# Kernel tuning notes

Hardware: AMD Instinct MI355X
Metric: run time of the kernel (lower is better)

Reference implementation:

```python
import jax, jax.numpy as jnp
import numpy as np

N = 100000
E = 3200000
D_IN = 128
D_OUT = 128


def setup_inputs() -> dict:
    key = jax.random.key(0)
    k1, k2, k3, k4, k5, k6, k7 = jax.random.split(key, 7)
    stdv = 1.0 / np.sqrt(D_OUT)
    x = jax.random.normal(k1, (N, D_IN), dtype=jnp.float32)
    rows = jax.random.randint(k2, (E,), 0, N, dtype=jnp.int32)
    cols = jax.random.randint(k3, (E,), 0, N, dtype=jnp.int32)
    edge_w = jax.random.uniform(k4, (E,), dtype=jnp.float32)
    W = jax.random.uniform(k5, (D_IN, D_OUT), minval=-stdv, maxval=stdv, dtype=jnp.float32)
    W_skip = jax.random.uniform(k6, (D_IN, D_OUT), minval=-stdv, maxval=stdv, dtype=jnp.float32)
    b = jax.random.uniform(k7, (D_OUT,), minval=-stdv, maxval=stdv, dtype=jnp.float32)
    return {"x": x, "rows": rows, "cols": cols, "edge_w": edge_w,
            "W": W, "W_skip": W_skip, "b": b}


def reference(x, rows, cols, edge_w, W, W_skip, b):
    # support1 = x @ W  [N, D_OUT]
    support1 = jnp.dot(x, W)
    # spmm(norm_adj, support1): out[r] = sum_{(r,c) in E} w_rc * support1[c]
    msgs = support1[cols] * edge_w[:, None]          # [E, D_OUT] gather
    agg = jax.ops.segment_sum(msgs, rows, num_segments=N)  # [N, D_OUT] scatter-add
    # skip connection + bias
    out = agg + jnp.dot(x, W_skip) + b
    return out
```

## Files before the change

### kernel.cpp

```cpp
#include <hip/hip_runtime.h>

#define D 128
#define BP_LOG 7
#define ROWS_H 64
#define MAX_NB 1024
#define GEMM_GRID 784
#define CHUNK_LOG 12
#define CAP 2560

typedef short bf16x8 __attribute__((ext_vector_type(8)));
typedef float f32x4  __attribute__((ext_vector_type(4)));

static __device__ __forceinline__ unsigned short f2bf(float f) {
    unsigned u = __float_as_uint(f);
    u += 0x7FFFu + ((u >> 16) & 1u);
    return (unsigned short)(u >> 16);
}

__global__ __launch_bounds__(256) void wconv_kernel(
    const float* __restrict__ W, const float* __restrict__ Ws,
    short* __restrict__ Wt, int* __restrict__ bhist, int nb)
{
    const int idx = blockIdx.x * 256 + threadIdx.x;
    if (idx < 2 * D * D) {
        const int mat = idx >> 14;
        const int rem = idx & (D * D - 1);
        const int n = rem >> 7, k = rem & (D - 1);
        const float* src = mat ? Ws : W;
        Wt[idx] = (short)f2bf(src[k * D + n]);
    }
    if (idx < nb) bhist[idx] = 0;
}

__global__ __launch_bounds__(256) void bhist_kernel(
    const int* __restrict__ rows, int* __restrict__ bhist, int E, int nb)
{
    __shared__ int h[MAX_NB];
    const int t = threadIdx.x;
    for (int i = t; i < nb; i += 256) h[i] = 0;
    __syncthreads();

    int i = blockIdx.x * 256 + t;
    const int stride = gridDim.x * 256;
    for (; i < E; i += stride) atomicAdd(&h[rows[i] >> BP_LOG], 1);
    __syncthreads();

    for (int i2 = t; i2 < nb; i2 += 256) {
        const int c = h[i2];
        if (c) atomicAdd(&bhist[i2], c);
    }
}

__global__ __launch_bounds__(256) void bscan_kernel(
    const int* __restrict__ bhist, int* __restrict__ bptr,
    int* __restrict__ bcur, int nb)
{
    const int t = threadIdx.x;
    const int base_i = t * 4;
    int v[4];
    int s = 0;
#pragma unroll
    for (int k = 0; k < 4; ++k) {
        v[k] = (base_i + k < nb) ? bhist[base_i + k] : 0;
        s += v[k];
    }

    const int lane = t & 63, wv = t >> 6;
    int sc = s;
    for (int o = 1; o < 64; o <<= 1) {
        const int u = __shfl_up(sc, o, 64);
        if (lane >= o) sc += u;
    }
    __shared__ int wsum[4];
    if (lane == 63) wsum[wv] = sc;
    __syncthreads();

    int wbase = 0;
    for (int w2 = 0; w2 < wv; ++w2) wbase += wsum[w2];
    int excl = wbase + (sc - s);
#pragma unroll
    for (int k = 0; k < 4; ++k) {
        if (base_i + k < nb) { bptr[base_i + k] = excl; bcur[base_i + k] = excl; }
        excl += v[k];
    }
    if (t == 255) bptr[nb] = wsum[0] + wsum[1] + wsum[2] + wsum[3];
}

__global__ __launch_bounds__(256) void gemm_part_kernel(
    const float* __restrict__ x, const short* __restrict__ Wt,
    const float* __restrict__ b, unsigned short* __restrict__ s1b,
    unsigned short* __restrict__ skipb, int N,
    const int* __restrict__ rows, const int* __restrict__ cols,
    const float* __restrict__ ew, int* __restrict__ bcur,
    int2* __restrict__ se1, int E, int nb)
{
    __shared__ short sx[64 * D];

    const int t = threadIdx.x;

    if (blockIdx.x >= GEMM_GRID) {
        int* h = (int*)sx;
        const int nbl = gridDim.x - GEMM_GRID;
        const int nchunks = (E + (1 << CHUNK_LOG) - 1) >> CHUNK_LOG;

        for (int c = blockIdx.x - GEMM_GRID; c < nchunks; c += nbl) {
            const int ebeg = c << CHUNK_LOG;
            const int eend = min(ebeg + (1 << CHUNK_LOG), E);

            for (int i = t; i < nb; i += 256) h[i] = 0;
            __syncthreads();

            for (int e = ebeg + t; e < eend; e += 256)
                atomicAdd(&h[rows[e] >> BP_LOG], 1);
            __syncthreads();

            for (int i = t; i < nb; i += 256) {
                const int cnt = h[i];
                h[i] = cnt ? atomicAdd(&bcur[i], cnt) : 0;
            }
            __syncthreads();

            for (int e = ebeg + t; e < eend; e += 256) {
                const int r    = rows[e];
                const int bkt  = r >> BP_LOG;
                const int slot = atomicAdd(&h[bkt], 1);
                se1[slot] = make_int2(((r & 127) << 20) | cols[e],
                                      __float_as_int(ew[e]));
            }
            __syncthreads();
        }
        return;
    }

    const int lane = t & 63;
    const int w    = t >> 6;

    const int bmat = w >> 1;
    const int bn0  = (w & 1) * 64 + (lane & 15);
    const int bk0  = (lane >> 4) * 8;
    bf16x8 Bf[4][4];
#pragma unroll
    for (int nf = 0; nf < 4; ++nf)
#pragma unroll
        for (int ks = 0; ks < 4; ++ks)
            Bf[nf][ks] = *(const bf16x8*)&Wt[
                ((size_t)bmat * D + bn0 + nf * 16) * D + ks * 32 + bk0];

    float bias[4];
#pragma unroll
    for (int nf = 0; nf < 4; ++nf)
        bias[nf] = (w >= 2) ? b[(w - 2) * 64 + nf * 16 + (lane & 15)] : 0.f;

    const int ntiles = (N + 63) >> 6;
    const int trow = t >> 2;
    const int tk   = (t & 3) * 4;

    for (int rt = blockIdx.x; rt < ntiles; rt += GEMM_GRID) {
        const int r0 = rt << 6;
        __syncthreads();

        const int grow = min(r0 + trow, N - 1);
        const float* xrow = &x[(size_t)grow * D];
#pragma unroll
        for (int i = 0; i < 8; ++i) {
            const int k = tk + i * 16;
            const float4 v = *(const float4*)&xrow[k];
            const unsigned lo = (unsigned)f2bf(v.x) | ((unsigned)f2bf(v.y) << 16);
            const unsigned hi = (unsigned)f2bf(v.z) | ((unsigned)f2bf(v.w) << 16);
            unsigned byte = trow * 256 + k * 2;
            byte ^= (unsigned)((trow & 7) << 4);
            *(uint2*)((char*)sx + byte) = make_uint2(lo, hi);
        }
        __syncthreads();

        f32x4 acc[4][4];
#pragma unroll
        for (int mf = 0; mf < 4; ++mf)
#pragma unroll
            for (int nf = 0; nf < 4; ++nf)
                acc[mf][nf] = (f32x4){0.f, 0.f, 0.f, 0.f};

#pragma unroll
        for (int ks = 0; ks < 4; ++ks) {
            bf16x8 Af[4];
#pragma unroll
            for (int mf = 0; mf < 4; ++mf) {
                const int row = mf * 16 + (lane & 15);
                unsigned byte = row * 256 + (ks * 32 + bk0) * 2;
                byte ^= (unsigned)((row & 7) << 4);
                Af[mf] = *(const bf16x8*)((const char*)sx + byte);
            }
#pragma unroll
            for (int mf = 0; mf < 4; ++mf)
#pragma unroll
                for (int nf = 0; nf < 4; ++nf)
                    acc[mf][nf] = __builtin_amdgcn_mfma_f32_16x16x32_bf16(
                        Af[mf], Bf[nf][ks], acc[mf][nf], 0, 0, 0);
        }

#pragma unroll
        for (int mf = 0; mf < 4; ++mf) {
#pragma unroll
            for (int i = 0; i < 4; ++i) {
                const int row = r0 + mf * 16 + (lane >> 4) * 4 + i;
                if (row < N) {
                    if (w < 2) {
#pragma unroll
                        for (int nf = 0; nf < 4; ++nf) {
                            const int col = w * 64 + nf * 16 + (lane & 15);
                            s1b[(size_t)row * D + col] = f2bf(acc[mf][nf][i]);
                        }
                    } else {
#pragma unroll
                        for (int nf = 0; nf < 4; ++nf) {
                            const int col = (w - 2) * 64 + nf * 16 + (lane & 15);
                            skipb[(size_t)row * D + col] =
                                f2bf(acc[mf][nf][i] + bias[nf]);
                        }
                    }
                }
            }
        }
    }
}

__global__ __launch_bounds__(512) void sortspmm_kernel(
    const unsigned short* __restrict__ s1b,
    const unsigned short* __restrict__ skipb,
    const int* __restrict__ bptr, const int2* __restrict__ se1,
    float* __restrict__ out, int N)
{
    __shared__ long long recs[CAP];
    __shared__ unsigned short perm[CAP];
    __shared__ int rpos[ROWS_H];
    __shared__ int rcur[ROWS_H];
    __shared__ int nstage;

    const int t    = threadIdx.x;
    const int lane = t & 63;
    const int wv   = t >> 6;
    const int sb   = blockIdx.x >> 1;
    const int hh   = blockIdx.x & 1;
    const int r0   = (sb << BP_LOG) + (hh << 6);
    const int j    = lane * 2;

    const int beg  = bptr[sb];
    const int end  = bptr[sb + 1];
    const long long* seq = (const long long*)se1;

    if (t < ROWS_H) rcur[t] = 0;
    if (t == 0) nstage = 0;
    __syncthreads();

    for (int e = beg + t; e < end; e += 512) {
        const long long rec = seq[e];
        const int rl = (int)((unsigned)rec >> 20);
        const bool m = ((rl >> 6) == hh);
        const unsigned long long bal = __ballot(m);
        if (bal) {
            const int leader = (int)__ffsll((long long)bal) - 1;
            int base = 0;
            if (lane == leader) base = atomicAdd(&nstage, __popcll(bal));
            base = __shfl(base, leader, 64);
            if (m) {
                const int slot = base +
                    (int)__popcll(bal & ((1ull << lane) - 1ull));
                if (slot < CAP) recs[slot] = rec;
            }
        }
    }
    __syncthreads();
    const int hcnt = nstage;

    if (hcnt <= CAP) {
        for (int i = t; i < hcnt; i += 512)
            atomicAdd(&rcur[(int)((unsigned)recs[i] >> 20) & 63], 1);
        __syncthreads();

        if (t < ROWS_H) {
            const int v = rcur[t];
            int sc = v;
#pragma unroll
            for (int o = 1; o < 64; o <<= 1) {
                const int u = __shfl_up(sc, o, 64);
                if (lane >= o) sc += u;
            }
            rpos[t] = sc - v;
            rcur[t] = sc - v;
        }
        __syncthreads();

        for (int i = t; i < hcnt; i += 512) {
            const int rl = (int)((unsigned)recs[i] >> 20) & 63;
            perm[atomicAdd(&rcur[rl], 1)] = (unsigned short)i;
        }
        __syncthreads();

        for (int i2 = 0; i2 < 8; ++i2) {
            const int rr = wv * 8 + i2;
            const int r  = r0 + rr;
            if (r >= N) break;
            int p        = rpos[rr];
            const int pe = rcur[rr];

            float2 acc = make_float2(0.f, 0.f);
            for (; p + 8 <= pe; p += 8) {
                int idx[8];
#pragma unroll
                for (int k = 0; k < 8; ++k) idx[k] = perm[p + k];
                long long ed[8];
#pragma unroll
                for (int k = 0; k < 8; ++k) ed[k] = recs[idx[k]];
                unsigned pk[8];
#pragma unroll
                for (int k = 0; k < 8; ++k)
                    pk[k] = *(const unsigned*)&s1b[
                        (size_t)((unsigned)ed[k] & 0xFFFFFu) * D + j];
#pragma unroll
                for (int k = 0; k < 8; ++k) {
                    const float w = __int_as_float((int)(ed[k] >> 32));
                    acc.x = fmaf(w, __uint_as_float(pk[k] << 16), acc.x);
                    acc.y = fmaf(w, __uint_as_float(pk[k] & 0xFFFF0000u), acc.y);
                }
            }
            for (; p < pe; ++p) {
                const long long ed = recs[perm[p]];
                const unsigned pk = *(const unsigned*)&s1b[
                    (size_t)((unsigned)ed & 0xFFFFFu) * D + j];
                const float w = __int_as_float((int)(ed >> 32));
                acc.x = fmaf(w, __uint_as_float(pk << 16), acc.x);
                acc.y = fmaf(w, __uint_as_float(pk & 0xFFFF0000u), acc.y);
            }

            const unsigned sk = *(const unsigned*)&skipb[(size_t)r * D + j];
            float2 o;
            o.x = acc.x + __uint_as_float(sk << 16);
            o.y = acc.y + __uint_as_float(sk & 0xFFFF0000u);
            *(float2*)&out[(size_t)r * D + j] = o;
        }
    } else {
        const int nr = min(ROWS_H, N - r0);
        for (int idx = t; idx < nr * 64; idx += 512) {
            const int rr = idx >> 6;
            const int cc = (idx & 63) * 2;
            const unsigned sk = *(const unsigned*)&skipb[(size_t)(r0 + rr) * D + cc];
            *(float2*)&out[(size_t)(r0 + rr) * D + cc] =
                make_float2(__uint_as_float(sk << 16),
                            __uint_as_float(sk & 0xFFFF0000u));
        }
        __syncthreads();

        for (int e = beg + wv; e < end; e += 8) {
            const long long ed = seq[e];
            const unsigned key = (unsigned)ed;
            const int rl = (int)(key >> 20);
            if ((rl >> 6) != hh) continue;
            const float w = __int_as_float((int)(ed >> 32));
            const unsigned pk = *(const unsigned*)&s1b[
                (size_t)(key & 0xFFFFFu) * D + j];
            float* op = &out[(size_t)(r0 + (rl & 63)) * D + j];
            unsafeAtomicAdd(op,     w * __uint_as_float(pk << 16));
            unsafeAtomicAdd(op + 1, w * __uint_as_float(pk & 0xFFFF0000u));
        }
    }
}

__global__ __launch_bounds__(512) void dual_gemm_fb_kernel(
    const float* __restrict__ x, const float* __restrict__ W,
    const float* __restrict__ Ws, const float* __restrict__ b,
    unsigned short* __restrict__ s1b, float* __restrict__ out, int N)
{
    __shared__ float sW[D * D];
    __shared__ float sWs[D * D];

    const int t = threadIdx.x;
    for (int i = t * 4; i < D * D; i += 512 * 4) {
        *(float4*)&sW[i]  = *(const float4*)&W[i];
        *(float4*)&sWs[i] = *(const float4*)&Ws[i];
    }
    __syncthreads();

    const int lane   = t & 63;
    const int wave   = blockIdx.x * 8 + (t >> 6);
    const int nwaves = gridDim.x * 8;
    const int j      = lane * 2;
    const float2 bb  = *(const float2*)&b[j];

    for (int r0 = wave * 4; r0 < N; r0 += nwaves * 4) {
        float2 xr[4];
#pragma unroll
        for (int r = 0; r < 4; ++r)
            xr[r] = *(const float2*)&x[(size_t)(r0 + r) * D + j];

        float2 a1[4], a2[4];
#pragma unroll
        for (int r = 0; r < 4; ++r) {
            a1[r] = make_float2(0.f, 0.f);
            a2[r] = make_float2(0.f, 0.f);
        }

#pragma unroll 8
        for (int k = 0; k < D; ++k) {
            const float2 wk  = *(const float2*)&sW[k * D + j];
            const float2 wsk = *(const float2*)&sWs[k * D + j];
#pragma unroll
            for (int r = 0; r < 4; ++r) {
                const float xv = __shfl((k & 1) ? xr[r].y : xr[r].x, k >> 1, 64);
                a1[r].x = fmaf(xv, wk.x,  a1[r].x);
                a1[r].y = fmaf(xv, wk.y,  a1[r].y);
                a2[r].x = fmaf(xv, wsk.x, a2[r].x);
                a2[r].y = fmaf(xv, wsk.y, a2[r].y);
            }
        }

#pragma unroll
        for (int r = 0; r < 4; ++r) {
            const unsigned pk = (unsigned)f2bf(a1[r].x) |
                                ((unsigned)f2bf(a1[r].y) << 16);
            *(unsigned*)&s1b[(size_t)(r0 + r) * D + j] = pk;
            *(float2*)&out[(size_t)(r0 + r) * D + j] =
                make_float2(a2[r].x + bb.x, a2[r].y + bb.y);
        }
    }
}

__global__ __launch_bounds__(256) void spmm_edges_kernel(
    const unsigned short* __restrict__ s1b, const int* __restrict__ rows,
    const int* __restrict__ cols, const float* __restrict__ ew,
    float* __restrict__ out, int E)
{
    const int lane = threadIdx.x & 63;
    const int wave = blockIdx.x * (blockDim.x >> 6) + (threadIdx.x >> 6);
    const int nw   = gridDim.x * (blockDim.x >> 6);
    const int j    = lane * 2;

    const int epw   = (E + nw - 1) / nw;
    const int e_beg = wave * epw;
    const int e_end = min(e_beg + epw, E);

    for (int e = e_beg; e < e_end; ++e) {
        const int   r = rows[e];
        const int   c = cols[e];
        const float w = ew[e];
        const unsigned p = *(const unsigned*)&s1b[(size_t)c * D + j];
        float* o = &out[(size_t)r * D + j];
        unsafeAtomicAdd(o,     w * __uint_as_float(p << 16));
        unsafeAtomicAdd(o + 1, w * __uint_as_float(p & 0xFFFF0000u));
    }
}

extern "C" void kernel_launch(void* const* d_in, const int* in_sizes, int n_in,
                              void* d_out, int out_size, void* d_ws, size_t ws_size,
                              hipStream_t stream) {
    const float* x    = (const float*)d_in[0];
    const int*   rows = (const int*)  d_in[1];
    const int*   cols = (const int*)  d_in[2];
    const float* ew   = (const float*)d_in[3];
    const float* W    = (const float*)d_in[4];
    const float* Ws   = (const float*)d_in[5];
    const float* b    = (const float*)d_in[6];
    float*       out  = (float*)d_out;

    const int N  = in_sizes[0] / D;
    const int E  = in_sizes[1];
    const int nb = (N + 127) >> BP_LOG;

    const size_t s1_bytes   = ((size_t)N * D * 2 + 15) & ~(size_t)15;
    const size_t skip_bytes = s1_bytes;
    const size_t wt_bytes   = (size_t)2 * D * D * 2;
    const size_t int_bytes  = (((size_t)(3 * nb + 1)) * 4 + 7) & ~(size_t)7;
    const size_t need       = s1_bytes + skip_bytes + wt_bytes + int_bytes
                              + (size_t)E * 8;

    unsigned short* s1b = (unsigned short*)d_ws;

    if (ws_size >= need && nb <= MAX_NB) {
        unsigned short* skipb = (unsigned short*)((char*)d_ws + s1_bytes);
        short* Wt    = (short*)((char*)d_ws + s1_bytes + skip_bytes);
        int*   ibase = (int*)((char*)d_ws + s1_bytes + skip_bytes + wt_bytes);
        int*  bhist  = ibase;
        int*  bptr   = ibase + nb;
        int*  bcur   = ibase + 2 * nb + 1;
        int2* se1    = (int2*)((char*)d_ws + s1_bytes + skip_bytes + wt_bytes
                               + int_bytes);

        wconv_kernel<<<(2 * D * D + 255) / 256, 256, 0, stream>>>(W, Ws, Wt, bhist, nb);
        bhist_kernel<<<512, 256, 0, stream>>>(rows, bhist, E, nb);
        bscan_kernel<<<1, 256, 0, stream>>>(bhist, bptr, bcur, nb);

        const int nchunks = (E + (1 << CHUNK_LOG) - 1) >> CHUNK_LOG;
        const int part_blocks = min(nchunks, 1024);
        gemm_part_kernel<<<GEMM_GRID + part_blocks, 256, 0, stream>>>(
            x, Wt, b, s1b, skipb, N, rows, cols, ew, bcur, se1, E, nb);

        sortspmm_kernel<<<nb * 2, 512, 0, stream>>>(s1b, skipb, bptr, se1, out, N);
    } else {
        dual_gemm_fb_kernel<<<768, 512, 0, stream>>>(x, W, Ws, b, s1b, (float*)d_out, N);
        spmm_edges_kernel<<<2048, 256, 0, stream>>>(s1b, rows, cols, ew, (float*)d_out, E);
    }
}
```

Measured before the change: 219.5 us.

## Reorder fused gemm/partition grid, vectorize histogram loads, unroll gather by 16

The fused GEMM+edge-partition kernel now puts the partition blocks first and gives each 64-row GEMM tile its own block instead of looping over a fixed grid, so the latency-bound partition work is dispatched early. The bucket histogram reads rows as int4 to cut load instructions. The SpMM gather loop gains a 16-wide unrolled stage for more loads in flight. The trade-off is more GEMM blocks each reloading the B fragments, and more register pressure in the gather loop.

Result: slower. 230.9 us (+5.2%).

```diff
diff --git a/kernel.cpp b/kernel.cpp
--- a/kernel.cpp
+++ b/kernel.cpp
@@ -4,7 +4,6 @@
 #define BP_LOG 7
 #define ROWS_H 64
 #define MAX_NB 1024
-#define GEMM_GRID 784
 #define CHUNK_LOG 12
 #define CAP 2560
 
@@ -40,9 +39,18 @@
     for (int i = t; i < nb; i += 256) h[i] = 0;
     __syncthreads();
 
+    const int nq = E >> 2;
     int i = blockIdx.x * 256 + t;
     const int stride = gridDim.x * 256;
-    for (; i < E; i += stride) atomicAdd(&h[rows[i] >> BP_LOG], 1);
+    for (; i < nq; i += stride) {
+        const int4 r4 = ((const int4*)rows)[i];
+        atomicAdd(&h[r4.x >> BP_LOG], 1);
+        atomicAdd(&h[r4.y >> BP_LOG], 1);
+        atomicAdd(&h[r4.z >> BP_LOG], 1);
+        atomicAdd(&h[r4.w >> BP_LOG], 1);
+    }
+    for (int e = (nq << 2) + blockIdx.x * 256 + t; e < E; e += stride)
+        atomicAdd(&h[rows[e] >> BP_LOG], 1);
     __syncthreads();
 
     for (int i2 = t; i2 < nb; i2 += 256) {
@@ -92,18 +100,17 @@
     unsigned short* __restrict__ skipb, int N,
     const int* __restrict__ rows, const int* __restrict__ cols,
     const float* __restrict__ ew, int* __restrict__ bcur,
-    int2* __restrict__ se1, int E, int nb)
+    int2* __restrict__ se1, int E, int nb, int part_grid)
 {
     __shared__ short sx[64 * D];
 
     const int t = threadIdx.x;
 
-    if (blockIdx.x >= GEMM_GRID) {
+    if (blockIdx.x < part_grid) {
         int* h = (int*)sx;
-        const int nbl = gridDim.x - GEMM_GRID;
         const int nchunks = (E + (1 << CHUNK_LOG) - 1) >> CHUNK_LOG;
 
-        for (int c = blockIdx.x - GEMM_GRID; c < nchunks; c += nbl) {
+        for (int c = blockIdx.x; c < nchunks; c += part_grid) {
             const int ebeg = c << CHUNK_LOG;
             const int eend = min(ebeg + (1 << CHUNK_LOG), E);
 
@@ -151,14 +158,12 @@
     for (int nf = 0; nf < 4; ++nf)
         bias[nf] = (w >= 2) ? b[(w - 2) * 64 + nf * 16 + (lane & 15)] : 0.f;
 
-    const int ntiles = (N + 63) >> 6;
+    const int rt = blockIdx.x - part_grid;
+    const int r0 = rt << 6;
     const int trow = t >> 2;
     const int tk   = (t & 3) * 4;
 
-    for (int rt = blockIdx.x; rt < ntiles; rt += GEMM_GRID) {
-        const int r0 = rt << 6;
-        __syncthreads();
-
+    {
         const int grow = min(r0 + trow, N - 1);
         const float* xrow = &x[(size_t)grow * D];
 #pragma unroll
@@ -304,6 +309,25 @@
             const int pe = rcur[rr];
 
             float2 acc = make_float2(0.f, 0.f);
+            for (; p + 16 <= pe; p += 16) {
+                int idx[16];
+#pragma unroll
+                for (int k = 0; k < 16; ++k) idx[k] = perm[p + k];
+                long long ed[16];
+#pragma unroll
+                for (int k = 0; k < 16; ++k) ed[k] = recs[idx[k]];
+                unsigned pk[16];
+#pragma unroll
+                for (int k = 0; k < 16; ++k)
+                    pk[k] = *(const unsigned*)&s1b[
+                        (size_t)((unsigned)ed[k] & 0xFFFFFu) * D + j];
+#pragma unroll
+                for (int k = 0; k < 16; ++k) {
+                    const float w = __int_as_float((int)(ed[k] >> 32));
+                    acc.x = fmaf(w, __uint_as_float(pk[k] << 16), acc.x);
+                    acc.y = fmaf(w, __uint_as_float(pk[k] & 0xFFFF0000u), acc.y);
+                }
+            }
             for (; p + 8 <= pe; p += 8) {
                 int idx[8];
 #pragma unroll
@@ -488,10 +512,11 @@
         bhist_kernel<<<512, 256, 0, stream>>>(rows, bhist, E, nb);
         bscan_kernel<<<1, 256, 0, stream>>>(bhist, bptr, bcur, nb);
 
-        const int nchunks = (E + (1 << CHUNK_LOG) - 1) >> CHUNK_LOG;
-        const int part_blocks = min(nchunks, 1024);
-        gemm_part_kernel<<<GEMM_GRID + part_blocks, 256, 0, stream>>>(
-            x, Wt, b, s1b, skipb, N, rows, cols, ew, bcur, se1, E, nb);
+        const int nchunks   = (E + (1 << CHUNK_LOG) - 1) >> CHUNK_LOG;
+        const int part_grid = min(nchunks, 1024);
+        const int ntiles    = (N + 63) >> 6;
+        gemm_part_kernel<<<part_grid + ntiles, 256, 0, stream>>>(
+            x, Wt, b, s1b, skipb, N, rows, cols, ew, bcur, se1, E, nb, part_grid);
 
         sortspmm_kernel<<<nb * 2, 512, 0, stream>>>(s1b, skipb, bptr, se1, out, N);
     } else {
```

## Replace histogram+scan bucketing with fixed-capacity buckets and overflow list

Applied to the files above, without the earlier changes.

Drops the separate histogram and prefix-scan kernels by giving each row bucket a fixed-capacity slot region (BCAP entries). Edges beyond capacity go to a global overflow array, which every SpMM block scans and applies with atomics. This removes two launches and a full pass over rows, at the cost of a larger, sparser workspace. Every block now also loops over the overflow count, which is expensive if the overflow grows large. Edges beyond OCAP are silently dropped.

Measured after the change: 200.0 us. -8.9%, faster.

```diff
diff --git a/kernel.cpp b/kernel.cpp
--- a/kernel.cpp
+++ b/kernel.cpp
@@ -7,6 +7,8 @@
 #define GEMM_GRID 784
 #define CHUNK_LOG 12
 #define CAP 2560
+#define BCAP 4864
+#define OCAP 32768
 
 typedef short bf16x8 __attribute__((ext_vector_type(8)));
 typedef float f32x4  __attribute__((ext_vector_type(4)));
@@ -19,7 +21,7 @@
 
 __global__ __launch_bounds__(256) void wconv_kernel(
     const float* __restrict__ W, const float* __restrict__ Ws,
-    short* __restrict__ Wt, int* __restrict__ bhist, int nb)
+    short* __restrict__ Wt, int* __restrict__ bcnt, int nb)
 {
     const int idx = blockIdx.x * 256 + threadIdx.x;
     if (idx < 2 * D * D) {
@@ -29,61 +31,7 @@
         const float* src = mat ? Ws : W;
         Wt[idx] = (short)f2bf(src[k * D + n]);
     }
-    if (idx < nb) bhist[idx] = 0;
-}
-
-__global__ __launch_bounds__(256) void bhist_kernel(
-    const int* __restrict__ rows, int* __restrict__ bhist, int E, int nb)
-{
-    __shared__ int h[MAX_NB];
-    const int t = threadIdx.x;
-    for (int i = t; i < nb; i += 256) h[i] = 0;
-    __syncthreads();
-
-    int i = blockIdx.x * 256 + t;
-    const int stride = gridDim.x * 256;
-    for (; i < E; i += stride) atomicAdd(&h[rows[i] >> BP_LOG], 1);
-    __syncthreads();
-
-    for (int i2 = t; i2 < nb; i2 += 256) {
-        const int c = h[i2];
-        if (c) atomicAdd(&bhist[i2], c);
-    }
-}
-
-__global__ __launch_bounds__(256) void bscan_kernel(
-    const int* __restrict__ bhist, int* __restrict__ bptr,
-    int* __restrict__ bcur, int nb)
-{
-    const int t = threadIdx.x;
-    const int base_i = t * 4;
-    int v[4];
-    int s = 0;
-#pragma unroll
-    for (int k = 0; k < 4; ++k) {
-        v[k] = (base_i + k < nb) ? bhist[base_i + k] : 0;
-        s += v[k];
-    }
-
-    const int lane = t & 63, wv = t >> 6;
-    int sc = s;
-    for (int o = 1; o < 64; o <<= 1) {
-        const int u = __shfl_up(sc, o, 64);
-        if (lane >= o) sc += u;
-    }
-    __shared__ int wsum[4];
-    if (lane == 63) wsum[wv] = sc;
-    __syncthreads();
-
-    int wbase = 0;
-    for (int w2 = 0; w2 < wv; ++w2) wbase += wsum[w2];
-    int excl = wbase + (sc - s);
-#pragma unroll
-    for (int k = 0; k < 4; ++k) {
-        if (base_i + k < nb) { bptr[base_i + k] = excl; bcur[base_i + k] = excl; }
-        excl += v[k];
-    }
-    if (t == 255) bptr[nb] = wsum[0] + wsum[1] + wsum[2] + wsum[3];
+    if (idx <= nb) bcnt[idx] = 0;
 }
 
 __global__ __launch_bounds__(256) void gemm_part_kernel(
@@ -91,8 +39,8 @@
     const float* __restrict__ b, unsigned short* __restrict__ s1b,
     unsigned short* __restrict__ skipb, int N,
     const int* __restrict__ rows, const int* __restrict__ cols,
-    const float* __restrict__ ew, int* __restrict__ bcur,
-    int2* __restrict__ se1, int E, int nb)
+    const float* __restrict__ ew, int* __restrict__ bcnt,
+    int2* __restrict__ se1, int4* __restrict__ ovf, int E, int nb)
 {
     __shared__ short sx[64 * D];
 
@@ -100,6 +48,7 @@
 
     if (blockIdx.x >= GEMM_GRID) {
         int* h = (int*)sx;
+        int* ocur = &bcnt[nb];
         const int nbl = gridDim.x - GEMM_GRID;
         const int nchunks = (E + (1 << CHUNK_LOG) - 1) >> CHUNK_LOG;
 
@@ -116,7 +65,7 @@
 
             for (int i = t; i < nb; i += 256) {
                 const int cnt = h[i];
-                h[i] = cnt ? atomicAdd(&bcur[i], cnt) : 0;
+                h[i] = cnt ? atomicAdd(&bcnt[i], cnt) : 0;
             }
             __syncthreads();
 
@@ -124,8 +73,16 @@
                 const int r    = rows[e];
                 const int bkt  = r >> BP_LOG;
                 const int slot = atomicAdd(&h[bkt], 1);
-                se1[slot] = make_int2(((r & 127) << 20) | cols[e],
-                                      __float_as_int(ew[e]));
+                if (slot < BCAP) {
+                    se1[(size_t)bkt * BCAP + slot] =
+                        make_int2(((r & 127) << 20) | cols[e],
+                                  __float_as_int(ew[e]));
+                } else {
+                    const int oi = atomicAdd(ocur, 1);
+                    if (oi < OCAP)
+                        ovf[oi] = make_int4(r, cols[e],
+                                            __float_as_int(ew[e]), 0);
+                }
             }
             __syncthreads();
         }
@@ -227,8 +184,8 @@
 __global__ __launch_bounds__(512) void sortspmm_kernel(
     const unsigned short* __restrict__ s1b,
     const unsigned short* __restrict__ skipb,
-    const int* __restrict__ bptr, const int2* __restrict__ se1,
-    float* __restrict__ out, int N)
+    const int* __restrict__ bcnt, const int2* __restrict__ se1,
+    const int4* __restrict__ ovf, float* __restrict__ out, int N, int nb)
 {
     __shared__ long long recs[CAP];
     __shared__ unsigned short perm[CAP];
@@ -244,8 +201,8 @@
     const int r0   = (sb << BP_LOG) + (hh << 6);
     const int j    = lane * 2;
 
-    const int beg  = bptr[sb];
-    const int end  = bptr[sb + 1];
+    const int beg  = sb * BCAP;
+    const int end  = beg + min(bcnt[sb], BCAP);
     const long long* seq = (const long long*)se1;
 
     if (t < ROWS_H) rcur[t] = 0;
@@ -363,6 +320,18 @@
             unsafeAtomicAdd(op + 1, w * __uint_as_float(pk & 0xFFFF0000u));
         }
     }
+
+    __syncthreads();
+    const int novf = min(bcnt[nb], OCAP);
+    for (int i = t >> 6; i < novf; i += 8) {
+        const int4 rec = ovf[i];
+        if ((rec.x >> BP_LOG) != sb || (((rec.x >> 6) & 1) != hh)) continue;
+        const float w = __int_as_float(rec.z);
+        const unsigned pk = *(const unsigned*)&s1b[(size_t)rec.y * D + j];
+        float* op = &out[(size_t)rec.x * D + j];
+        unsafeAtomicAdd(op,     w * __uint_as_float(pk << 16));
+        unsafeAtomicAdd(op + 1, w * __uint_as_float(pk & 0xFFFF0000u));
+    }
 }
 
 __global__ __launch_bounds__(512) void dual_gemm_fb_kernel(
@@ -468,32 +437,32 @@
     const size_t s1_bytes   = ((size_t)N * D * 2 + 15) & ~(size_t)15;
     const size_t skip_bytes = s1_bytes;
     const size_t wt_bytes   = (size_t)2 * D * D * 2;
-    const size_t int_bytes  = (((size_t)(3 * nb + 1)) * 4 + 7) & ~(size_t)7;
+    const size_t int_bytes  = (((size_t)(nb + 1)) * 4 + 15) & ~(size_t)15;
+    const size_t ovf_bytes  = (size_t)OCAP * 16;
+    const size_t se1_bytes  = (size_t)nb * BCAP * 8;
     const size_t need       = s1_bytes + skip_bytes + wt_bytes + int_bytes
-                              + (size_t)E * 8;
+                              + ovf_bytes + se1_bytes;
 
     unsigned short* s1b = (unsigned short*)d_ws;
 
     if (ws_size >= need && nb <= MAX_NB) {
         unsigned short* skipb = (unsigned short*)((char*)d_ws + s1_bytes);
-        short* Wt    = (short*)((char*)d_ws + s1_bytes + skip_bytes);
-        int*   ibase = (int*)((char*)d_ws + s1_bytes + skip_bytes + wt_bytes);
-        int*  bhist  = ibase;
-        int*  bptr   = ibase + nb;
-        int*  bcur   = ibase + 2 * nb + 1;
-        int2* se1    = (int2*)((char*)d_ws + s1_bytes + skip_bytes + wt_bytes
-                               + int_bytes);
-
-        wconv_kernel<<<(2 * D * D + 255) / 256, 256, 0, stream>>>(W, Ws, Wt, bhist, nb);
-        bhist_kernel<<<512, 256, 0, stream>>>(rows, bhist, E, nb);
-        bscan_kernel<<<1, 256, 0, stream>>>(bhist, bptr, bcur, nb);
+        short* Wt   = (short*)((char*)d_ws + s1_bytes + skip_bytes);
+        int*   bcnt = (int*)((char*)d_ws + s1_bytes + skip_bytes + wt_bytes);
+        int4*  ovf  = (int4*)((char*)d_ws + s1_bytes + skip_bytes + wt_bytes
+                              + int_bytes);
+        int2*  se1  = (int2*)((char*)d_ws + s1_bytes + skip_bytes + wt_bytes
+                              + int_bytes + ovf_bytes);
+
+        wconv_kernel<<<(2 * D * D + 255) / 256, 256, 0, stream>>>(W, Ws, Wt, bcnt, nb);
 
         const int nchunks = (E + (1 << CHUNK_LOG) - 1) >> CHUNK_LOG;
         const int part_blocks = min(nchunks, 1024);
         gemm_part_kernel<<<GEMM_GRID + part_blocks, 256, 0, stream>>>(
-            x, Wt, b, s1b, skipb, N, rows, cols, ew, bcur, se1, E, nb);
-
-        sortspmm_kernel<<<nb * 2, 512, 0, stream>>>(s1b, skipb, bptr, se1, out, N);
+            x, Wt, b, s1b, skipb, N, rows, cols, ew, bcnt, se1, ovf, E, nb);
+
+        sortspmm_kernel<<<nb * 2, 512, 0, stream>>>(
+            s1b, skipb, bcnt, se1, ovf, out, N, nb);
     } else {
         dual_gemm_fb_kernel<<<768, 512, 0, stream>>>(x, W, Ws, b, s1b, (float*)d_out, N);
         spmm_edges_kernel<<<2048, 256, 0, stream>>>(s1b, rows, cols, ew, (float*)d_out, E);
```
